# Optimization experiments

Measured on AMD Instinct MI355X. Metric: run time of the kernel, lower is better.

Reference implementation:

```python
import jax, jax.numpy as jnp
import numpy as np

N_INT, N_LANE, N_SENS, N_INJ = 50000, 100000, 50000, 20000
H = 128
L = 3

def setup_inputs() -> dict:
    key = jax.random.key(0)
    ks = jax.random.split(key, 24)
    def edges(k1, k2, n_src, n_tgt, e):
        return jnp.stack([
            jax.random.randint(k1, (e,), 0, n_src),
            jax.random.randint(k2, (e,), 0, n_tgt),
        ]).astype(jnp.int64)
    return {
        "x_int":  jax.random.normal(ks[0], (N_INT, 32), jnp.float32),
        "x_lane": jax.random.normal(ks[1], (N_LANE, 16), jnp.float32),
        "x_sens": jax.random.normal(ks[2], (N_SENS, 8), jnp.float32),
        "x_inj":  jax.random.normal(ks[3], (N_INJ, 8), jnp.float32),
        "edge_spatial":   edges(ks[4], ks[5], N_INT, N_INT, 640000),
        "edge_flow_lane": edges(ks[6], ks[7], N_LANE, N_INT, 640000),
        "edge_flow_sens": edges(ks[8], ks[9], N_SENS, N_INT, 320000),
        "edge_incident":  edges(ks[10], ks[11], N_INJ, N_INT, 160000),
        "W_int":  jax.random.normal(ks[12], (32, H), jnp.float32) * 0.1,
        "b_int":  jax.random.normal(ks[13], (H,), jnp.float32) * 0.1,
        "W_lane": jax.random.normal(ks[14], (16, H), jnp.float32) * 0.1,
        "b_lane": jax.random.normal(ks[15], (H,), jnp.float32) * 0.1,
        "W_sens": jax.random.normal(ks[16], (8, H), jnp.float32) * 0.1,
        "b_sens": jax.random.normal(ks[17], (H,), jnp.float32) * 0.1,
        "W_inj":  jax.random.normal(ks[18], (8, H), jnp.float32) * 0.1,
        "b_inj":  jax.random.normal(ks[19], (H,), jnp.float32) * 0.1,
        "self_W": jax.random.normal(ks[20], (L, H, H), jnp.float32) * 0.05,
        "self_b": jax.random.normal(ks[21], (L, H), jnp.float32) * 0.05,
        "rel_W":  jax.random.normal(ks[22], (L, H, H), jnp.float32) * 0.05,
    }

def _relation(src_feat, edge_index, num_targets, W):
    # gather -> linear (no bias) -> scatter-mean onto int-node targets
    msg = src_feat[edge_index[0]] @ W                      # [E, H]
    s = jax.ops.segment_sum(msg, edge_index[1], num_segments=num_targets)
    cnt = jax.ops.segment_sum(jnp.ones((edge_index.shape[1], 1), msg.dtype),
                              edge_index[1], num_segments=num_targets)
    return s / jnp.clip(cnt, 1.0)

def reference(x_int, x_lane, x_sens, x_inj,
              edge_spatial, edge_flow_lane, edge_flow_sens, edge_incident,
              W_int, b_int, W_lane, b_lane, W_sens, b_sens, W_inj, b_inj,
              self_W, self_b, rel_W):
    h_int = x_int @ W_int + b_int
    h_lane = x_lane @ W_lane + b_lane
    h_sens = x_sens @ W_sens + b_sens
    h_inj = x_inj @ W_inj + b_inj
    n = h_int.shape[0]
    for l in range(self_W.shape[0]):
        W = rel_W[l]
        spatial = _relation(h_int, edge_spatial, n, W)
        flow_l = _relation(h_lane, edge_flow_lane, n, W)
        flow_s = _relation(h_sens, edge_flow_sens, n, W)
        inc = _relation(h_inj, edge_incident, n, W)
        h_int = jax.nn.elu(h_int @ self_W[l] + self_b[l] + spatial + flow_l + flow_s + inc)
    return h_int
```

## Files before the change

kernel.cpp:

```cpp
#include <hip/hip_runtime.h>
#include <hip/hip_bf16.h>
#include <math.h>

#define H 128
#define SB 64
#define NCP 8

typedef float f32x4 __attribute__((ext_vector_type(4)));
typedef __bf16 bf16x8 __attribute__((ext_vector_type(8)));

__device__ __forceinline__ unsigned short f2bf(float f) {
    return __builtin_bit_cast(unsigned short, (__bf16)f);
}
__device__ __forceinline__ unsigned pack2(float lo, float hi) {
    return (unsigned)f2bf(lo) | ((unsigned)f2bf(hi) << 16);
}
__device__ __forceinline__ void acc2(unsigned u, float& a, float& b) {
    union { unsigned u; float f; } x, y;
    x.u = u << 16; y.u = u & 0xffff0000u;
    a += x.f; b += y.f;
}
__device__ __forceinline__ float bflo(unsigned u) {
    union { unsigned u; float f; } x; x.u = u << 16; return x.f;
}
__device__ __forceinline__ float bfhi(unsigned u) {
    union { unsigned u; float f; } x; x.u = u & 0xffff0000u; return x.f;
}

__global__ __launch_bounds__(256) void k_count0(const int* __restrict__ s0, int E0,
                                                int* __restrict__ cnt, int* __restrict__ seq)
{
    int e = blockIdx.x * 256 + threadIdx.x;
    if (e >= E0) return;
    seq[e] = atomicAdd(&cnt[s0[E0 + e]], 1);
}

__global__ __launch_bounds__(256) void k_scan1(const int* __restrict__ cnt, int n,
                                               int* __restrict__ partial)
{
    int blk = blockIdx.x;
    int chunk = (n + SB - 1) / SB;
    int lo = blk * chunk, hi = min(lo + chunk, n);
    int s = 0;
    for (int i = lo + threadIdx.x; i < hi; i += 256) s += cnt[i];
    __shared__ int sh[256];
    sh[threadIdx.x] = s; __syncthreads();
    for (int d = 128; d; d >>= 1) {
        if (threadIdx.x < d) sh[threadIdx.x] += sh[threadIdx.x + d];
        __syncthreads();
    }
    if (threadIdx.x == 0) partial[blk] = sh[0];
}

__global__ __launch_bounds__(64) void k_scan2(int* __restrict__ partial,
                                              int* __restrict__ rowptr, int n, int E0)
{
    int lane = threadIdx.x;
    int v = partial[lane];
    int inc = v;
    for (int d = 1; d < 64; d <<= 1) {
        int t = __shfl_up(inc, d);
        if (lane >= d) inc += t;
    }
    partial[lane] = inc - v;
    if (lane == 0) rowptr[n] = E0;
}

__global__ __launch_bounds__(256) void k_scan3(const int* __restrict__ cnt,
                                               const int* __restrict__ partial,
                                               int* __restrict__ rowptr,
                                               float* __restrict__ recip, int n)
{
    int blk = blockIdx.x;
    int chunk = (n + SB - 1) / SB;
    int lo = blk * chunk, hi = min(lo + chunk, n);
    int per = (chunk + 255) >> 8;
    int tlo = min(lo + threadIdx.x * per, hi);
    int thi = min(tlo + per, hi);
    int s = 0;
    for (int i = tlo; i < thi; ++i) s += cnt[i];
    __shared__ int sh[256];
    sh[threadIdx.x] = s; __syncthreads();
    for (int d = 1; d < 256; d <<= 1) {
        int t = (threadIdx.x >= d) ? sh[threadIdx.x - d] : 0;
        __syncthreads();
        sh[threadIdx.x] += t;
        __syncthreads();
    }
    int run = partial[blk] + sh[threadIdx.x] - s;
    for (int i = tlo; i < thi; ++i) {
        int c = cnt[i];
        rowptr[i] = run;
        recip[i] = (c > 0) ? 1.0f / (float)c : 0.0f;
        run += c;
    }
}

__global__ __launch_bounds__(256) void k_fill_seq(const int* __restrict__ s0, int E0,
                                                  const int* __restrict__ rowptr,
                                                  const int* __restrict__ seq,
                                                  int* __restrict__ col)
{
    int e = blockIdx.x * 256 + threadIdx.x;
    if (e >= E0) return;
    int t = s0[E0 + e];
    col[rowptr[t] + seq[e]] = s0[e];
}

__global__ __launch_bounds__(256) void k_scatx_all(
    const int* __restrict__ s1, const int* __restrict__ s2, const int* __restrict__ s3,
    const float* __restrict__ xL, const float* __restrict__ xS, const float* __restrict__ xI,
    int E1, int E2, int E3, int b1, int b2,
    float* __restrict__ REP, size_t S, int n)
{
    float* R = REP + (size_t)(blockIdx.x & (NCP - 1)) * S;
    int b = blockIdx.x;
    if (b < b1) {
        int e = b * 16 + (threadIdx.x >> 4);
        if (e >= E1) return;
        int d = threadIdx.x & 15;
        int src = s1[e], tgt = s1[E1 + e];
        unsafeAtomicAdd(&R[(size_t)tgt * 16 + d], xL[(size_t)src * 16 + d]);
        if (d == 0) unsafeAtomicAdd(&R[(size_t)32 * n + tgt], 1.0f);
    } else if (b < b2) {
        b -= b1;
        int e = b * 32 + (threadIdx.x >> 3);
        if (e >= E2) return;
        int d = threadIdx.x & 7;
        int src = s2[e], tgt = s2[E2 + e];
        unsafeAtomicAdd(&R[(size_t)16 * n + (size_t)tgt * 8 + d], xS[(size_t)src * 8 + d]);
        if (d == 0) unsafeAtomicAdd(&R[(size_t)33 * n + tgt], 1.0f);
    } else {
        b -= b2;
        int e = b * 32 + (threadIdx.x >> 3);
        if (e >= E3) return;
        int d = threadIdx.x & 7;
        int src = s3[e], tgt = s3[E3 + e];
        unsafeAtomicAdd(&R[(size_t)24 * n + (size_t)tgt * 8 + d], xI[(size_t)src * 8 + d]);
        if (d == 0) unsafeAtomicAdd(&R[(size_t)34 * n + tgt], 1.0f);
    }
}

__global__ __launch_bounds__(256) void k_encmfma(const float* __restrict__ x,
                                                 const float* __restrict__ W,
                                                 const float* __restrict__ b,
                                                 unsigned short* __restrict__ h, int n)
{
    __shared__ __align__(16) char WB[128 * 80];
    int tid = threadIdx.x;
    {
        int c = tid & 127, khalf = tid >> 7;
        for (int kk = 0; kk < 16; ++kk) {
            int k = khalf * 16 + kk;
            *(unsigned short*)(WB + c * 80 + k * 2) = f2bf(W[(size_t)k * H + c]);
        }
    }
    int lane = tid & 63, wv = tid >> 6;
    int r16 = lane & 15, kgrp = lane >> 4;
    int rowbase = blockIdx.x * 64 + wv * 16;
    int arow = rowbase + r16; if (arow >= n) arow = n - 1;
    const float* xr = x + (size_t)arow * 32 + kgrp * 8;
    float4 xa = *(const float4*)xr, xb = *(const float4*)(xr + 4);
    bf16x8 af;
    af[0] = (__bf16)xa.x; af[1] = (__bf16)xa.y; af[2] = (__bf16)xa.z; af[3] = (__bf16)xa.w;
    af[4] = (__bf16)xb.x; af[5] = (__bf16)xb.y; af[6] = (__bf16)xb.z; af[7] = (__bf16)xb.w;
    __syncthreads();
#pragma unroll
    for (int ct = 0; ct < 8; ++ct) {
        int c = ct * 16 + r16;
        bf16x8 bf = *(const bf16x8*)(WB + c * 80 + kgrp * 16);
        f32x4 acc = { 0.f, 0.f, 0.f, 0.f };
        acc = __builtin_amdgcn_mfma_f32_16x16x32_bf16(af, bf, acc, 0, 0, 0);
        float bb = b[c];
#pragma unroll
        for (int i = 0; i < 4; ++i) {
            int grow = rowbase + kgrp * 4 + i;
            if (grow < n) h[(size_t)grow * H + c] = f2bf(acc[i] + bb);
        }
    }
}

__global__ __launch_bounds__(256) void k_stat(
    const float* __restrict__ REP, size_t S,
    const float* __restrict__ WL, const float* __restrict__ WSn, const float* __restrict__ WI,
    const float* __restrict__ bL, const float* __restrict__ bS, const float* __restrict__ bI,
    unsigned short* __restrict__ statb, int n)
{
    __shared__ float Wc[32][128];
    __shared__ float xs[8][32];
    __shared__ float msk[8][3];
    int t = threadIdx.x;
    for (int i = t; i < 16 * 128; i += 256) Wc[i >> 7][i & 127] = WL[i];
    for (int i = t; i < 8 * 128; i += 256)  Wc[16 + (i >> 7)][i & 127] = WSn[i];
    for (int i = t; i < 8 * 128; i += 256)  Wc[24 + (i >> 7)][i & 127] = WI[i];
    {
        int rr = t >> 5, k = t & 31;
        int rrow = blockIdx.x * 8 + rr; if (rrow >= n) rrow = n - 1;
        size_t voff, coff;
        if (k < 16)      { voff = (size_t)rrow * 16 + k;                 coff = (size_t)32 * n + rrow; }
        else if (k < 24) { voff = (size_t)16 * n + (size_t)rrow * 8 + (k - 16); coff = (size_t)33 * n + rrow; }
        else             { voff = (size_t)24 * n + (size_t)rrow * 8 + (k - 24); coff = (size_t)34 * n + rrow; }
        float v = 0.f, c = 0.f;
#pragma unroll
        for (int cp = 0; cp < NCP; ++cp) {
            v += REP[(size_t)cp * S + voff];
            c += REP[(size_t)cp * S + coff];
        }
        float r = (c > 0.f) ? 1.0f / c : 0.0f;
        xs[rr][k] = v * r;
        if (k == 0)  msk[rr][0] = (c > 0.f) ? 1.f : 0.f;
        if (k == 16) msk[rr][1] = (c > 0.f) ? 1.f : 0.f;
        if (k == 24) msk[rr][2] = (c > 0.f) ? 1.f : 0.f;
    }
    __syncthreads();
    int rl = t >> 5, c4 = (t & 31) << 2;
    int row = blockIdx.x * 8 + rl;
    float a0 = 0.f, a1 = 0.f, a2 = 0.f, a3 = 0.f;
#pragma unroll
    for (int k = 0; k < 32; ++k) {
        float xv = xs[rl][k];
        a0 += xv * Wc[k][c4 + 0]; a1 += xv * Wc[k][c4 + 1];
        a2 += xv * Wc[k][c4 + 2]; a3 += xv * Wc[k][c4 + 3];
    }
    if (row < n) {
        float mL = msk[rl][0], mS = msk[rl][1], mI = msk[rl][2];
        uint2 res;
        res.x = pack2(a0 + mL * bL[c4 + 0] + mS * bS[c4 + 0] + mI * bI[c4 + 0],
                      a1 + mL * bL[c4 + 1] + mS * bS[c4 + 1] + mI * bI[c4 + 1]);
        res.y = pack2(a2 + mL * bL[c4 + 2] + mS * bS[c4 + 2] + mI * bI[c4 + 2],
                      a3 + mL * bL[c4 + 3] + mS * bS[c4 + 3] + mI * bI[c4 + 3]);
        *(uint2*)(statb + (size_t)row * H + c4) = res;
    }
}

__global__ __launch_bounds__(256) void k_spmm(const unsigned short* __restrict__ hsrc,
                                              const int* __restrict__ rowptr,
                                              const int* __restrict__ col,
                                              const float* __restrict__ recip,
                                              const unsigned short* __restrict__ statb,
                                              unsigned short* __restrict__ aggout, int n)
{
    int row = blockIdx.x * 16 + (threadIdx.x >> 4);
    if (row >= n) return;
    int q = (threadIdx.x & 15) << 3;
    int beg = rowptr[row], end = rowptr[row + 1];

    float a0 = 0.f, a1 = 0.f, a2 = 0.f, a3 = 0.f, a4 = 0.f, a5 = 0.f, a6 = 0.f, a7 = 0.f;
    int e = beg;
    for (; e + 4 <= end; e += 4) {
        int s0 = col[e], s1 = col[e + 1], s2 = col[e + 2], s3 = col[e + 3];
        uint4 v0 = *(const uint4*)(hsrc + (size_t)s0 * H + q);
        uint4 v1 = *(const uint4*)(hsrc + (size_t)s1 * H + q);
        uint4 v2 = *(const uint4*)(hsrc + (size_t)s2 * H + q);
        uint4 v3 = *(const uint4*)(hsrc + (size_t)s3 * H + q);
        acc2(v0.x, a0, a1); acc2(v0.y, a2, a3); acc2(v0.z, a4, a5); acc2(v0.w, a6, a7);
        acc2(v1.x, a0, a1); acc2(v1.y, a2, a3); acc2(v1.z, a4, a5); acc2(v1.w, a6, a7);
        acc2(v2.x, a0, a1); acc2(v2.y, a2, a3); acc2(v2.z, a4, a5); acc2(v2.w, a6, a7);
        acc2(v3.x, a0, a1); acc2(v3.y, a2, a3); acc2(v3.z, a4, a5); acc2(v3.w, a6, a7);
    }
    for (; e < end; ++e) {
        uint4 v0 = *(const uint4*)(hsrc + (size_t)col[e] * H + q);
        acc2(v0.x, a0, a1); acc2(v0.y, a2, a3); acc2(v0.z, a4, a5); acc2(v0.w, a6, a7);
    }

    float r = recip[row];
    size_t o = (size_t)row * H + q;
    uint4 sv = *(const uint4*)(statb + o);
    uint4 w;
    w.x = pack2(a0 * r + bflo(sv.x), a1 * r + bfhi(sv.x));
    w.y = pack2(a2 * r + bflo(sv.y), a3 * r + bfhi(sv.y));
    w.z = pack2(a4 * r + bflo(sv.z), a5 * r + bfhi(sv.z));
    w.w = pack2(a6 * r + bflo(sv.w), a7 * r + bfhi(sv.w));
    *(uint4*)(aggout + o) = w;
}

template<int LAST>
__global__ __launch_bounds__(256) void k_layer(const unsigned short* __restrict__ hb,
                                               const unsigned short* __restrict__ aggb,
                                               const float* __restrict__ Ws,
                                               const float* __restrict__ Wr,
                                               const float* __restrict__ bias,
                                               unsigned short* __restrict__ hbout,
                                               float* __restrict__ fout, int n)
{
    __shared__ __align__(16) char BT[128 * 256 * 2];

    int tid = threadIdx.x;
    {
        int c = tid & 127, half = tid >> 7;
        for (int kc = half; kc < 32; kc += 2) {
            int kk0 = kc * 8;
            const float* Wsrc = (kk0 < 128) ? (Ws + (size_t)kk0 * H + c)
                                            : (Wr + (size_t)(kk0 - 128) * H + c);
            bf16x8 pack;
#pragma unroll
            for (int j = 0; j < 8; ++j) pack[j] = (__bf16)Wsrc[(size_t)j * H];
            int woff = c * 512 + ((kc * 16) ^ ((c & 7) << 4));
            *(bf16x8*)(BT + woff) = pack;
        }
    }

    int lane = tid & 63, wv = tid >> 6;
    int r16 = lane & 15, kgrp = lane >> 4;
    int rowbase = blockIdx.x * 64 + wv * 16;
    int arow = rowbase + r16; if (arow >= n) arow = n - 1;

    bf16x8 afrag[8];
#pragma unroll
    for (int ks = 0; ks < 8; ++ks) {
        int k0 = ks * 32 + kgrp * 8;
        const unsigned short* src = (k0 < 128) ? (hb + (size_t)arow * H + k0)
                                               : (aggb + (size_t)arow * H + (k0 - 128));
        afrag[ks] = *(const bf16x8*)src;
    }
    __syncthreads();

#pragma unroll
    for (int ct = 0; ct < 8; ++ct) {
        int c = ct * 16 + r16;
        f32x4 acc = { 0.f, 0.f, 0.f, 0.f };
#pragma unroll
        for (int ks = 0; ks < 8; ++ks) {
            int kbyte = ks * 64 + kgrp * 16;
            int off = c * 512 + (kbyte ^ ((c & 7) << 4));
            bf16x8 bfrag = *(const bf16x8*)(BT + off);
            acc = __builtin_amdgcn_mfma_f32_16x16x32_bf16(afrag[ks], bfrag, acc, 0, 0, 0);
        }
        float bb = bias[c];
#pragma unroll
        for (int i = 0; i < 4; ++i) {
            int grow = rowbase + kgrp * 4 + i;
            if (grow < n) {
                float v = acc[i] + bb;
                v = (v > 0.f) ? v : (expf(v) - 1.f);
                if (LAST) fout[(size_t)grow * H + c] = v;
                else      hbout[(size_t)grow * H + c] = f2bf(v);
            }
        }
    }
}

extern "C" void kernel_launch(void* const* d_in, const int* in_sizes, int n_in,
                              void* d_out, int out_size, void* d_ws, size_t ws_size,
                              hipStream_t stream)
{
    const float* x_int  = (const float*)d_in[0];
    const float* x_lane = (const float*)d_in[1];
    const float* x_sens = (const float*)d_in[2];
    const float* x_inj  = (const float*)d_in[3];
    const int*   e_sp   = (const int*)d_in[4];
    const int*   e_fl   = (const int*)d_in[5];
    const int*   e_fs   = (const int*)d_in[6];
    const int*   e_in   = (const int*)d_in[7];
    const float* W_int  = (const float*)d_in[8];
    const float* b_int  = (const float*)d_in[9];
    const float* W_lane = (const float*)d_in[10];
    const float* b_lane = (const float*)d_in[11];
    const float* W_sens = (const float*)d_in[12];
    const float* b_sens = (const float*)d_in[13];
    const float* W_inj  = (const float*)d_in[14];
    const float* b_inj  = (const float*)d_in[15];
    const float* self_W = (const float*)d_in[16];
    const float* self_b = (const float*)d_in[17];
    const float* rel_W  = (const float*)d_in[18];

    const int n = in_sizes[0] / 32;
    const int E0 = in_sizes[4] / 2, E1 = in_sizes[5] / 2, E2 = in_sizes[6] / 2, E3 = in_sizes[7] / 2;

    float* out = (float*)d_out;

    char* base = (char*)d_ws;
    size_t off = 0;
    auto carve = [&](size_t bytes) { char* p = base + off; off += (bytes + 15) & ~(size_t)15; return p; };
    unsigned short* hb_a  = (unsigned short*)carve((size_t)n * H * 2);
    unsigned short* hb_b  = (unsigned short*)carve((size_t)n * H * 2);
    unsigned short* aggb  = (unsigned short*)carve((size_t)n * H * 2);
    unsigned short* statb = (unsigned short*)carve((size_t)n * H * 2);
    const size_t S = (size_t)n * 35;
    float* REP  = (float*)carve(NCP * S * 4);
    int*   cnt0 = (int*)carve((size_t)n * 4);
    float* recip0 = (float*)carve((size_t)n * 4);
    int* rowptr  = (int*)carve((size_t)(n + 1) * 4);
    int* partial = (int*)carve((size_t)SB * 4);
    int* seq     = (int*)carve((size_t)E0 * 4);
    int* col0    = (int*)carve((size_t)E0 * 4);

    int B0 = (E0 + 255) / 256;

    hipMemsetAsync(REP, 0, NCP * S * 4, stream);
    hipMemsetAsync(cnt0, 0, (size_t)n * 4, stream);
    k_count0<<<B0, 256, 0, stream>>>(e_sp, E0, cnt0, seq);

    k_scan1<<<SB, 256, 0, stream>>>(cnt0, n, partial);
    k_scan2<<<1, 64, 0, stream>>>(partial, rowptr, n, E0);
    k_scan3<<<SB, 256, 0, stream>>>(cnt0, partial, rowptr, recip0, n);
    k_fill_seq<<<B0, 256, 0, stream>>>(e_sp, E0, rowptr, seq, col0);

    k_encmfma<<<(n + 63) / 64, 256, 0, stream>>>(x_int, W_int, b_int, hb_a, n);

    int SB1 = (E1 + 15) / 16, SB2 = (E2 + 31) / 32, SB3 = (E3 + 31) / 32;
    k_scatx_all<<<SB1 + SB2 + SB3, 256, 0, stream>>>(e_fl, e_fs, e_in, x_lane, x_sens, x_inj,
                                                     E1, E2, E3, SB1, SB1 + SB2, REP, S, n);
    k_stat<<<(n + 7) / 8, 256, 0, stream>>>(REP, S, W_lane, W_sens, W_inj,
                                            b_lane, b_sens, b_inj, statb, n);

    const int spmm_grid = (n + 15) / 16;
    const int layer_grid = (n + 63) / 64;
    unsigned short* cur = hb_a;
    unsigned short* nxt = hb_b;
    for (int l = 0; l < 3; ++l) {
        k_spmm<<<spmm_grid, 256, 0, stream>>>(cur, rowptr, col0, recip0, statb, aggb, n);
        const float* Ws = self_W + (size_t)l * H * H;
        const float* Wr = rel_W  + (size_t)l * H * H;
        const float* bb = self_b + (size_t)l * H;
        if (l == 2)
            k_layer<1><<<layer_grid, 256, 0, stream>>>(cur, aggb, Ws, Wr, bb, nullptr, out, n);
        else
            k_layer<0><<<layer_grid, 256, 0, stream>>>(cur, aggb, Ws, Wr, bb, nxt, nullptr, n);
        unsigned short* t = cur; cur = nxt; nxt = t;
    }
}
```

Measured before the change: 374.1 us.

## Fuse front-end scatter, count, and encoder kernels; use packed bf16 atomics

Merges the spatial-edge counting, the three static-relation scatters and the int-node encoder into one launch. The two tail steps, CSR column fill and static projection, become a second launch. The eight fp32 replica scatter buffers are replaced by single bf16 buffers updated with packed bf16 atomic adds, plus separate fp32 count arrays, all cleared by one small memset. This reduces launch count, memset size and atomic traffic. The cost is lower accumulation precision from summing in bf16 and more atomic contention on a single copy.

```diff
diff --git a/kernel.cpp b/kernel.cpp
--- a/kernel.cpp
+++ b/kernel.cpp
@@ -4,7 +4,6 @@
 
 #define H 128
 #define SB 64
-#define NCP 8
 
 typedef float f32x4 __attribute__((ext_vector_type(4)));
 typedef __bf16 bf16x8 __attribute__((ext_vector_type(8)));
@@ -14,6 +13,9 @@
 }
 __device__ __forceinline__ unsigned pack2(float lo, float hi) {
     return (unsigned)f2bf(lo) | ((unsigned)f2bf(hi) << 16);
+}
+__device__ __forceinline__ float bf2f(unsigned short u) {
+    return __builtin_bit_cast(float, (unsigned)u << 16);
 }
 __device__ __forceinline__ void acc2(unsigned u, float& a, float& b) {
     union { unsigned u; float f; } x, y;
@@ -26,13 +28,94 @@
 __device__ __forceinline__ float bfhi(unsigned u) {
     union { unsigned u; float f; } x; x.u = u & 0xffff0000u; return x.f;
 }
-
-__global__ __launch_bounds__(256) void k_count0(const int* __restrict__ s0, int E0,
-                                                int* __restrict__ cnt, int* __restrict__ seq)
-{
-    int e = blockIdx.x * 256 + threadIdx.x;
-    if (e >= E0) return;
-    seq[e] = atomicAdd(&cnt[s0[E0 + e]], 1);
+__device__ __forceinline__ void atom_pk_bf16(unsigned short* a, unsigned d) {
+    asm volatile("global_atomic_pk_add_bf16 %0, %1, off" :: "v"(a), "v"(d) : "memory");
+}
+
+__global__ __launch_bounds__(256) void k_front(
+    const int* __restrict__ s0, const int* __restrict__ s1,
+    const int* __restrict__ s2, const int* __restrict__ s3,
+    const float* __restrict__ xL, const float* __restrict__ xS, const float* __restrict__ xI,
+    const float* __restrict__ x_int, const float* __restrict__ W_int, const float* __restrict__ b_int,
+    int E0, int E1, int E2, int E3,
+    int g1, int g2, int g3, int g4,
+    unsigned short* __restrict__ XLb, unsigned short* __restrict__ XSb, unsigned short* __restrict__ XIb,
+    float* __restrict__ CNT1, float* __restrict__ CNT2, float* __restrict__ CNT3,
+    int* __restrict__ cnt0, int* __restrict__ seq,
+    unsigned short* __restrict__ hb, int n)
+{
+    __shared__ __align__(16) char WB[128 * 80];
+    int b = blockIdx.x;
+    int tid = threadIdx.x;
+
+    if (b < g1) {
+        int e = b * 32 + (tid >> 3);
+        if (e >= E1) return;
+        int p = tid & 7;
+        int src = s1[e], tgt = s1[E1 + e];
+        float2 v = *(const float2*)(xL + (size_t)src * 16 + 2 * p);
+        atom_pk_bf16(XLb + (size_t)tgt * 16 + 2 * p, pack2(v.x, v.y));
+        if (p == 0) unsafeAtomicAdd(&CNT1[tgt], 1.0f);
+        return;
+    }
+    if (b < g2) {
+        int e = (b - g1) * 64 + (tid >> 2);
+        if (e >= E2) return;
+        int p = tid & 3;
+        int src = s2[e], tgt = s2[E2 + e];
+        float2 v = *(const float2*)(xS + (size_t)src * 8 + 2 * p);
+        atom_pk_bf16(XSb + (size_t)tgt * 8 + 2 * p, pack2(v.x, v.y));
+        if (p == 0) unsafeAtomicAdd(&CNT2[tgt], 1.0f);
+        return;
+    }
+    if (b < g3) {
+        int e = (b - g2) * 64 + (tid >> 2);
+        if (e >= E3) return;
+        int p = tid & 3;
+        int src = s3[e], tgt = s3[E3 + e];
+        float2 v = *(const float2*)(xI + (size_t)src * 8 + 2 * p);
+        atom_pk_bf16(XIb + (size_t)tgt * 8 + 2 * p, pack2(v.x, v.y));
+        if (p == 0) unsafeAtomicAdd(&CNT3[tgt], 1.0f);
+        return;
+    }
+    if (b < g4) {
+        int e = (b - g3) * 256 + tid;
+        if (e >= E0) return;
+        seq[e] = atomicAdd(&cnt0[s0[E0 + e]], 1);
+        return;
+    }
+
+    int eb = b - g4;
+    {
+        int c = tid & 127, khalf = tid >> 7;
+        for (int kk = 0; kk < 16; ++kk) {
+            int k = khalf * 16 + kk;
+            *(unsigned short*)(WB + c * 80 + k * 2) = f2bf(W_int[(size_t)k * H + c]);
+        }
+    }
+    int lane = tid & 63, wv = tid >> 6;
+    int r16 = lane & 15, kgrp = lane >> 4;
+    int rowbase = eb * 64 + wv * 16;
+    int arow = rowbase + r16; if (arow >= n) arow = n - 1;
+    const float* xr = x_int + (size_t)arow * 32 + kgrp * 8;
+    float4 xa = *(const float4*)xr, xb = *(const float4*)(xr + 4);
+    bf16x8 af;
+    af[0] = (__bf16)xa.x; af[1] = (__bf16)xa.y; af[2] = (__bf16)xa.z; af[3] = (__bf16)xa.w;
+    af[4] = (__bf16)xb.x; af[5] = (__bf16)xb.y; af[6] = (__bf16)xb.z; af[7] = (__bf16)xb.w;
+    __syncthreads();
+#pragma unroll
+    for (int ct = 0; ct < 8; ++ct) {
+        int c = ct * 16 + r16;
+        bf16x8 bf = *(const bf16x8*)(WB + c * 80 + kgrp * 16);
+        f32x4 acc = { 0.f, 0.f, 0.f, 0.f };
+        acc = __builtin_amdgcn_mfma_f32_16x16x32_bf16(af, bf, acc, 0, 0, 0);
+        float bb = b_int[c];
+#pragma unroll
+        for (int i = 0; i < 4; ++i) {
+            int grow = rowbase + kgrp * 4 + i;
+            if (grow < n) hb[(size_t)grow * H + c] = f2bf(acc[i] + bb);
+        }
+    }
 }
 
 __global__ __launch_bounds__(256) void k_scan1(const int* __restrict__ cnt, int n,
@@ -96,92 +179,12 @@
     }
 }
 
-__global__ __launch_bounds__(256) void k_fill_seq(const int* __restrict__ s0, int E0,
-                                                  const int* __restrict__ rowptr,
-                                                  const int* __restrict__ seq,
-                                                  int* __restrict__ col)
-{
-    int e = blockIdx.x * 256 + threadIdx.x;
-    if (e >= E0) return;
-    int t = s0[E0 + e];
-    col[rowptr[t] + seq[e]] = s0[e];
-}
-
-__global__ __launch_bounds__(256) void k_scatx_all(
-    const int* __restrict__ s1, const int* __restrict__ s2, const int* __restrict__ s3,
-    const float* __restrict__ xL, const float* __restrict__ xS, const float* __restrict__ xI,
-    int E1, int E2, int E3, int b1, int b2,
-    float* __restrict__ REP, size_t S, int n)
-{
-    float* R = REP + (size_t)(blockIdx.x & (NCP - 1)) * S;
-    int b = blockIdx.x;
-    if (b < b1) {
-        int e = b * 16 + (threadIdx.x >> 4);
-        if (e >= E1) return;
-        int d = threadIdx.x & 15;
-        int src = s1[e], tgt = s1[E1 + e];
-        unsafeAtomicAdd(&R[(size_t)tgt * 16 + d], xL[(size_t)src * 16 + d]);
-        if (d == 0) unsafeAtomicAdd(&R[(size_t)32 * n + tgt], 1.0f);
-    } else if (b < b2) {
-        b -= b1;
-        int e = b * 32 + (threadIdx.x >> 3);
-        if (e >= E2) return;
-        int d = threadIdx.x & 7;
-        int src = s2[e], tgt = s2[E2 + e];
-        unsafeAtomicAdd(&R[(size_t)16 * n + (size_t)tgt * 8 + d], xS[(size_t)src * 8 + d]);
-        if (d == 0) unsafeAtomicAdd(&R[(size_t)33 * n + tgt], 1.0f);
-    } else {
-        b -= b2;
-        int e = b * 32 + (threadIdx.x >> 3);
-        if (e >= E3) return;
-        int d = threadIdx.x & 7;
-        int src = s3[e], tgt = s3[E3 + e];
-        unsafeAtomicAdd(&R[(size_t)24 * n + (size_t)tgt * 8 + d], xI[(size_t)src * 8 + d]);
-        if (d == 0) unsafeAtomicAdd(&R[(size_t)34 * n + tgt], 1.0f);
-    }
-}
-
-__global__ __launch_bounds__(256) void k_encmfma(const float* __restrict__ x,
-                                                 const float* __restrict__ W,
-                                                 const float* __restrict__ b,
-                                                 unsigned short* __restrict__ h, int n)
-{
-    __shared__ __align__(16) char WB[128 * 80];
-    int tid = threadIdx.x;
-    {
-        int c = tid & 127, khalf = tid >> 7;
-        for (int kk = 0; kk < 16; ++kk) {
-            int k = khalf * 16 + kk;
-            *(unsigned short*)(WB + c * 80 + k * 2) = f2bf(W[(size_t)k * H + c]);
-        }
-    }
-    int lane = tid & 63, wv = tid >> 6;
-    int r16 = lane & 15, kgrp = lane >> 4;
-    int rowbase = blockIdx.x * 64 + wv * 16;
-    int arow = rowbase + r16; if (arow >= n) arow = n - 1;
-    const float* xr = x + (size_t)arow * 32 + kgrp * 8;
-    float4 xa = *(const float4*)xr, xb = *(const float4*)(xr + 4);
-    bf16x8 af;
-    af[0] = (__bf16)xa.x; af[1] = (__bf16)xa.y; af[2] = (__bf16)xa.z; af[3] = (__bf16)xa.w;
-    af[4] = (__bf16)xb.x; af[5] = (__bf16)xb.y; af[6] = (__bf16)xb.z; af[7] = (__bf16)xb.w;
-    __syncthreads();
-#pragma unroll
-    for (int ct = 0; ct < 8; ++ct) {
-        int c = ct * 16 + r16;
-        bf16x8 bf = *(const bf16x8*)(WB + c * 80 + kgrp * 16);
-        f32x4 acc = { 0.f, 0.f, 0.f, 0.f };
-        acc = __builtin_amdgcn_mfma_f32_16x16x32_bf16(af, bf, acc, 0, 0, 0);
-        float bb = b[c];
-#pragma unroll
-        for (int i = 0; i < 4; ++i) {
-            int grow = rowbase + kgrp * 4 + i;
-            if (grow < n) h[(size_t)grow * H + c] = f2bf(acc[i] + bb);
-        }
-    }
-}
-
-__global__ __launch_bounds__(256) void k_stat(
-    const float* __restrict__ REP, size_t S,
+__global__ __launch_bounds__(256) void k_tail(
+    const int* __restrict__ s0, int E0,
+    const int* __restrict__ rowptr, const int* __restrict__ seq, int* __restrict__ col, int Bfill,
+    const unsigned short* __restrict__ XLb, const unsigned short* __restrict__ XSb,
+    const unsigned short* __restrict__ XIb,
+    const float* __restrict__ CNT1, const float* __restrict__ CNT2, const float* __restrict__ CNT3,
     const float* __restrict__ WL, const float* __restrict__ WSn, const float* __restrict__ WI,
     const float* __restrict__ bL, const float* __restrict__ bS, const float* __restrict__ bI,
     unsigned short* __restrict__ statb, int n)
@@ -189,32 +192,44 @@
     __shared__ float Wc[32][128];
     __shared__ float xs[8][32];
     __shared__ float msk[8][3];
+
+    int b = blockIdx.x;
     int t = threadIdx.x;
+    if (b < Bfill) {
+        int e = b * 256 + t;
+        if (e >= E0) return;
+        int tg = s0[E0 + e];
+        col[rowptr[tg] + seq[e]] = s0[e];
+        return;
+    }
+    int sb = b - Bfill;
+
     for (int i = t; i < 16 * 128; i += 256) Wc[i >> 7][i & 127] = WL[i];
     for (int i = t; i < 8 * 128; i += 256)  Wc[16 + (i >> 7)][i & 127] = WSn[i];
     for (int i = t; i < 8 * 128; i += 256)  Wc[24 + (i >> 7)][i & 127] = WI[i];
     {
         int rr = t >> 5, k = t & 31;
-        int rrow = blockIdx.x * 8 + rr; if (rrow >= n) rrow = n - 1;
-        size_t voff, coff;
-        if (k < 16)      { voff = (size_t)rrow * 16 + k;                 coff = (size_t)32 * n + rrow; }
-        else if (k < 24) { voff = (size_t)16 * n + (size_t)rrow * 8 + (k - 16); coff = (size_t)33 * n + rrow; }
-        else             { voff = (size_t)24 * n + (size_t)rrow * 8 + (k - 24); coff = (size_t)34 * n + rrow; }
-        float v = 0.f, c = 0.f;
-#pragma unroll
-        for (int cp = 0; cp < NCP; ++cp) {
-            v += REP[(size_t)cp * S + voff];
-            c += REP[(size_t)cp * S + coff];
+        int rrow = sb * 8 + rr; if (rrow >= n) rrow = n - 1;
+        float v, c;
+        if (k < 16) {
+            c = CNT1[rrow];
+            v = bf2f(XLb[(size_t)rrow * 16 + k]);
+            if (k == 0) msk[rr][0] = (c > 0.f) ? 1.f : 0.f;
+        } else if (k < 24) {
+            c = CNT2[rrow];
+            v = bf2f(XSb[(size_t)rrow * 8 + (k - 16)]);
+            if (k == 16) msk[rr][1] = (c > 0.f) ? 1.f : 0.f;
+        } else {
+            c = CNT3[rrow];
+            v = bf2f(XIb[(size_t)rrow * 8 + (k - 24)]);
+            if (k == 24) msk[rr][2] = (c > 0.f) ? 1.f : 0.f;
         }
         float r = (c > 0.f) ? 1.0f / c : 0.0f;
         xs[rr][k] = v * r;
-        if (k == 0)  msk[rr][0] = (c > 0.f) ? 1.f : 0.f;
-        if (k == 16) msk[rr][1] = (c > 0.f) ? 1.f : 0.f;
-        if (k == 24) msk[rr][2] = (c > 0.f) ? 1.f : 0.f;
     }
     __syncthreads();
     int rl = t >> 5, c4 = (t & 31) << 2;
-    int row = blockIdx.x * 8 + rl;
+    int row = sb * 8 + rl;
     float a0 = 0.f, a1 = 0.f, a2 = 0.f, a3 = 0.f;
 #pragma unroll
     for (int k = 0; k < 32; ++k) {
@@ -376,33 +391,44 @@
     unsigned short* hb_b  = (unsigned short*)carve((size_t)n * H * 2);
     unsigned short* aggb  = (unsigned short*)carve((size_t)n * H * 2);
     unsigned short* statb = (unsigned short*)carve((size_t)n * H * 2);
-    const size_t S = (size_t)n * 35;
-    float* REP  = (float*)carve(NCP * S * 4);
-    int*   cnt0 = (int*)carve((size_t)n * 4);
+    char* Z = carve((size_t)n * 80);
+    unsigned short* XLb = (unsigned short*)Z;
+    unsigned short* XSb = XLb + (size_t)n * 16;
+    unsigned short* XIb = XSb + (size_t)n * 8;
+    float* CNT1 = (float*)(XIb + (size_t)n * 8);
+    float* CNT2 = CNT1 + n;
+    float* CNT3 = CNT2 + n;
+    int*   cnt0 = (int*)(CNT3 + n);
     float* recip0 = (float*)carve((size_t)n * 4);
     int* rowptr  = (int*)carve((size_t)(n + 1) * 4);
     int* partial = (int*)carve((size_t)SB * 4);
     int* seq     = (int*)carve((size_t)E0 * 4);
     int* col0    = (int*)carve((size_t)E0 * 4);
 
-    int B0 = (E0 + 255) / 256;
-
-    hipMemsetAsync(REP, 0, NCP * S * 4, stream);
-    hipMemsetAsync(cnt0, 0, (size_t)n * 4, stream);
-    k_count0<<<B0, 256, 0, stream>>>(e_sp, E0, cnt0, seq);
+    int G1 = (E1 + 31) / 32;
+    int G2 = (E2 + 63) / 64;
+    int G3 = (E3 + 63) / 64;
+    int G4 = (E0 + 255) / 256;
+    int G5 = (n + 63) / 64;
+    int g1 = G1, g2 = g1 + G2, g3 = g2 + G3, g4 = g3 + G4;
+
+    hipMemsetAsync(Z, 0, (size_t)n * 80, stream);
+    k_front<<<g4 + G5, 256, 0, stream>>>(e_sp, e_fl, e_fs, e_in, x_lane, x_sens, x_inj,
+                                         x_int, W_int, b_int,
+                                         E0, E1, E2, E3, g1, g2, g3, g4,
+                                         XLb, XSb, XIb, CNT1, CNT2, CNT3,
+                                         cnt0, seq, hb_a, n);
 
     k_scan1<<<SB, 256, 0, stream>>>(cnt0, n, partial);
     k_scan2<<<1, 64, 0, stream>>>(partial, rowptr, n, E0);
     k_scan3<<<SB, 256, 0, stream>>>(cnt0, partial, rowptr, recip0, n);
-    k_fill_seq<<<B0, 256, 0, stream>>>(e_sp, E0, rowptr, seq, col0);
-
-    k_encmfma<<<(n + 63) / 64, 256, 0, stream>>>(x_int, W_int, b_int, hb_a, n);
-
-    int SB1 = (E1 + 15) / 16, SB2 = (E2 + 31) / 32, SB3 = (E3 + 31) / 32;
-    k_scatx_all<<<SB1 + SB2 + SB3, 256, 0, stream>>>(e_fl, e_fs, e_in, x_lane, x_sens, x_inj,
-                                                     E1, E2, E3, SB1, SB1 + SB2, REP, S, n);
-    k_stat<<<(n + 7) / 8, 256, 0, stream>>>(REP, S, W_lane, W_sens, W_inj,
-                                            b_lane, b_sens, b_inj, statb, n);
+
+    int Bfill = (E0 + 255) / 256;
+    int Bstat = (n + 7) / 8;
+    k_tail<<<Bfill + Bstat, 256, 0, stream>>>(e_sp, E0, rowptr, seq, col0, Bfill,
+                                              XLb, XSb, XIb, CNT1, CNT2, CNT3,
+                                              W_lane, W_sens, W_inj,
+                                              b_lane, b_sens, b_inj, statb, n);
 
     const int spmm_grid = (n + 15) / 16;
     const int layer_grid = (n + 63) / 64;
```

Measured after the change: 359.6 us. 3.9% less time.
